# Performance work log

Measured on AMD Instinct MI355X. Metric: run time of the kernel, lower is better.

Reference implementation:

```python
import jax, jax.numpy as jnp
import numpy as np

T, B, N, L = 4, 8, 25000, 64
D_IN = 1 + 2 * L  # node_dim + latent + time_dim


def setup_inputs() -> dict:
    key = jax.random.key(0)
    ks = jax.random.split(key, 20)
    f = lambda k, shp, s=0.1: jax.random.normal(k, shp, dtype=jnp.float32) * s
    z = lambda shp: jnp.zeros(shp, jnp.float32)
    return dict(
        raw=f(ks[0], (T, B, N, 1), 1.0),
        r_label=f(ks[1], (T, B, N, 1), 1.0),
        t=jax.random.uniform(ks[2], (T, B, N, 1), dtype=jnp.float32) * 100.0,
        src=jax.random.randint(ks[3], (T, B), 0, N, dtype=jnp.int32),
        tar=jax.random.randint(ks[4], (T, B), 0, N, dtype=jnp.int32),
        n_mask=jax.random.randint(ks[5], (T, B, N), 0, 2, dtype=jnp.int32),
        w_t=f(ks[6], (L,)), b_t=f(ks[7], (L,)),
        W_msg=f(ks[8], (1 + L, L)), b_msg=z((L,)),
        Wi=f(ks[9], (L, 3 * L)), Wh=f(ks[10], (L, 3 * L)),
        bi=z((3 * L,)), bh=z((3 * L,)),
        Wq=f(ks[11], (D_IN, L)), bq=z((L,)),
        Wk=f(ks[12], (D_IN, L)), bk=z((L,)),
        Wv=f(ks[13], (D_IN, L)), bv=z((L,)),
        W_out=f(ks[14], (L, 1)), b_out=z((1,)),
    )


def reference(raw, r_label, t, src, tar, n_mask, w_t, b_t, W_msg, b_msg,
              Wi, Wh, bi, bh, Wq, bq, Wk, bk, Wv, bv, W_out, b_out):
    Ldim = w_t.shape[0]
    Bdim, Ndim = raw.shape[1], raw.shape[2]
    bidx = jnp.arange(Bdim)
    scale = 1.0 / jnp.sqrt(jnp.float32(Ldim))
    enc0 = jnp.cos(b_t)  # time encoding of t=0 for the target query

    def time_enc(tt):  # [..., 1] -> [..., L]
        return jnp.cos(tt * w_t + b_t)

    def gru(x, h):  # torch.nn.GRUCell math
        gi = x @ Wi + bi
        gh = h @ Wh + bh
        ir, iz, inn = jnp.split(gi, 3, axis=-1)
        hr, hz, hn = jnp.split(gh, 3, axis=-1)
        rg = jax.nn.sigmoid(ir + hr)
        zg = jax.nn.sigmoid(iz + hz)
        ng = jnp.tanh(inn + rg * hn)
        return (1.0 - zg) * ng + zg * h

    def step(carry, inp):
        memory, r = carry            # [N,L], [B,N,1]
        t_b, tar_b, mask_b, rlab_b = inp  # [B,N,1], [B], [B,N], [N,1]
        enc_t = time_enc(t_b)        # [B,N,L]
        # 1. memory update (message from last batch element, GRU over all nodes)
        msg = jnp.concatenate([r[-1], enc_t[-1]], axis=-1) @ W_msg + b_msg  # [N,L]
        mem2 = gru(msg, memory)      # [N,L]
        # 2. embedding: target query over all node features
        tar_r = r[bidx, tar_b]       # [B,1]
        tar_hid = mem2[tar_b]        # [B,L]
        tar_h = jnp.concatenate(
            [tar_r, tar_hid, jnp.broadcast_to(enc0, (Bdim, Ldim))], axis=-1)  # [B,1+2L]
        h = jnp.concatenate(
            [r, jnp.broadcast_to(mem2[None], (Bdim, Ndim, Ldim)), enc_t], axis=-1)  # [B,N,1+2L]
        q = tar_h @ Wq + bq          # [B,L]
        k = h @ Wk + bk              # [B,N,L]
        v = h @ Wv + bv              # [B,N,L]
        scores = jnp.einsum('bl,bnl->bn', q, k) * scale
        scores = jnp.where(mask_b > 0, scores, jnp.float32(-1e9))
        attn = jax.nn.softmax(scores, axis=-1)
        z = jnp.einsum('bn,bnl->bl', attn, v)  # [B,L]
        logit = z @ W_out + b_out    # [B,1]
        # vectorized scatter replacing the python loop r_pred[tar_id]=pred_logit
        r_pred = r[-1].at[tar_b].set(logit)    # [N,1]
        r_last = 0.5 * (r_pred + rlab_b)       # teacher forcing blend
        r_next = jnp.broadcast_to(r_last[None], (Bdim, Ndim, 1))
        return (mem2, r_next), logit

    mem0 = jnp.zeros((Ndim, Ldim), jnp.float32)
    rlab_last = r_label[:, -1]  # [T,N,1]
    (_, _), logits = jax.lax.scan(step, (mem0, raw[0]), (t, tar, n_mask, rlab_last))
    return logits  # [T,B,1]
```

## Files before the change

### kernel.cpp

```cpp
#include <hip/hip_runtime.h>
#include <math.h>

#define TSTEPS 4
#define BB 8
#define NN 25000
#define LLD 64
#define DIN 129

#define OFF_W6    0
#define OFF_I4    24576
#define OFF_R4    24832
#define OFF_A     25088
#define OFF_WQ0   33473
#define OFF_CA    33602
#define OFF_C0Q   33667
#define OFF_WVO   33668
#define OFF_C0    33797
#define OFF_WQC   33856
#define OFF_BFRAG 36864
#define OFF_MEMA  73728
#define OFF_MEMB  1673728
#define OFF_RLAST 3273728
#define OFF_PART  3298728
#define NBLK 98
#define PSTRIDE 132

typedef short s16x8 __attribute__((ext_vector_type(8)));
typedef float f32x4 __attribute__((ext_vector_type(4)));

__device__ __forceinline__ float sigm(float x) { return 1.f / (1.f + __expf(-x)); }
__device__ __forceinline__ float tanh_fast(float x) {
  float ax = fabsf(x);
  float e = __expf(-2.f * ax);
  float t = (1.f - e) / (1.f + e);
  return copysignf(t, x);
}
__device__ __forceinline__ float wred_max(float v) {
#pragma unroll
  for (int m = 32; m; m >>= 1) v = fmaxf(v, __shfl_xor(v, m));
  return v;
}
__device__ __forceinline__ float wred_sum(float v) {
#pragma unroll
  for (int m = 32; m; m >>= 1) v += __shfl_xor(v, m);
  return v;
}
__device__ __forceinline__ unsigned short bf16_rne(float v) {
  unsigned int u = __float_as_uint(v);
  unsigned int r = (u + 0x7FFFu + ((u >> 16) & 1u)) >> 16;
  return (unsigned short)r;
}
__device__ __forceinline__ float bf16_to_f(unsigned short b) {
  return __uint_as_float(((unsigned int)b) << 16);
}

__global__ __launch_bounds__(1024) void k_setup(
    const float* __restrict__ W_msg, const float* __restrict__ Wi,
    const float* __restrict__ bi, const float* __restrict__ b_msg,
    const float* __restrict__ bh, const float* __restrict__ Wh,
    const float* __restrict__ Wq, const float* __restrict__ bq,
    const float* __restrict__ Wk, const float* __restrict__ bk,
    const float* __restrict__ Wv, const float* __restrict__ bv,
    const float* __restrict__ W_out, const float* __restrict__ b_out,
    const float* __restrict__ b_t, float* __restrict__ ws) {
  if (blockIdx.x == 0) {
    __shared__ float u_lds[64];
    int tid = threadIdx.x;
    if (tid < 64) {
      float acc = bq[tid];
      for (int l = 0; l < 64; l++) acc += __cosf(b_t[l]) * Wq[(65 + l) * 64 + tid];
      u_lds[tid] = acc;
    }
    __syncthreads();
    if (tid < 129) {
      float acc = 0.f;
      for (int j = 0; j < 64; j++) acc += Wk[tid * 64 + j] * u_lds[j];
      ws[OFF_WQ0 + tid] = acc;
    } else if (tid == 129) {
      float acc = 0.f;
      for (int j = 0; j < 64; j++) acc += bk[j] * u_lds[j];
      ws[OFF_C0Q] = acc;
    }
    return;
  }
  int id = (blockIdx.x - 1) * 1024 + threadIdx.x;
  if (id < 24576) {
    int k = id / 384, rem = id % 384, l = rem / 6, g = rem % 6;
    float acc = 0.f;
    if (g < 3) {
      for (int m = 0; m < 64; m++) acc += W_msg[(k + 1) * 64 + m] * Wi[m * 192 + g * 64 + l];
    } else {
      acc = Wh[k * 192 + (g - 3) * 64 + l];
    }
    ws[OFF_W6 + id] = acc;
  } else if (id < 24832) {
    int id2 = id - 24576, l = id2 / 4, g = id2 % 4;
    float v;
    if (g == 3) v = bh[128 + l];
    else {
      int j = g * 64 + l;
      float bcf = bi[j];
      for (int m = 0; m < 64; m++) bcf += b_msg[m] * Wi[m * 192 + j];
      v = (g < 2) ? (bcf + bh[j]) : bcf;
    }
    ws[OFF_I4 + id2] = v;
  } else if (id < 25088) {
    int id2 = id - 24832, l = id2 / 4, g = id2 % 4;
    float v = 0.f;
    if (g < 3) {
      for (int m = 0; m < 64; m++) v += W_msg[m] * Wi[m * 192 + g * 64 + l];
    }
    ws[OFF_R4 + id2] = v;
  } else if (id < 33473) {
    int id3 = id - 25088, d = id3 / 65, i = id3 % 65;
    float acc = 0.f;
    for (int j = 0; j < 64; j++) acc += Wk[d * 64 + j] * Wq[i * 64 + j];
    ws[OFF_A + id3] = acc;
  } else if (id < 33538) {
    int i = id - 33473;
    float acc = 0.f;
    for (int j = 0; j < 64; j++) acc += bk[j] * Wq[i * 64 + j];
    ws[OFF_CA + i] = acc;
  } else if (id < 33667) {
    int d = id - 33538;
    float acc = 0.f;
    for (int j = 0; j < 64; j++) acc += Wv[d * 64 + j] * W_out[j];
    ws[OFF_WVO + d] = acc;
  } else if (id == 33667) {
    float acc = b_out[0];
    for (int j = 0; j < 64; j++) acc += bv[j] * W_out[j];
    ws[OFF_C0] = acc;
  }
}

__global__ __launch_bounds__(1024) void k_pack(
    const float* __restrict__ ws_r, float* __restrict__ ws) {
  int id = blockIdx.x * 1024 + threadIdx.x;
  int r = id & 7, lane = (id >> 3) & 63, kt = (id >> 9) & 3, ct = id >> 11;
  int col = 16 * ct + (lane & 15);
  int k = 32 * kt + ((lane >> 4) << 3) + r;
  int a = col >> 6, l = col & 63;
  float w = 0.f;
  if (k < 64) {
    if (a < 3) w = ws_r[OFF_W6 + (k * 64 + l) * 6 + a];
  } else {
    int k2 = k - 64;
    if (a == 0) w = ws_r[OFF_W6 + (k2 * 64 + l) * 6 + 3];
    else if (a == 1) w = ws_r[OFF_W6 + (k2 * 64 + l) * 6 + 4];
    else if (a == 3) w = ws_r[OFF_W6 + (k2 * 64 + l) * 6 + 5];
  }
  unsigned short hb = bf16_rne(w);
  unsigned short lb = bf16_rne(w - bf16_to_f(hb));
  unsigned short* BFu = (unsigned short*)(ws + OFF_BFRAG);
  int idx = ((ct * 4 + kt) * 64 + lane) * 8 + r;
  BFu[idx] = hb;
  BFu[32768 + idx] = lb;
}

__global__ __launch_bounds__(256, 2) void k_gru(
    const float* __restrict__ t_in, const float* __restrict__ raw,
    const float* __restrict__ r_in, const float* __restrict__ w_t,
    const float* __restrict__ b_t, const float* __restrict__ i4p,
    const float* __restrict__ r4p, const unsigned short* __restrict__ BF,
    const float* __restrict__ memPrev, float* __restrict__ memNext,
    const int* __restrict__ tar, const float* __restrict__ A,
    const float* __restrict__ wq0, const float* __restrict__ cA,
    const float* __restrict__ c0q, float* __restrict__ wqc, int tt) {
  __shared__ unsigned short XhiS[64 * 136];
  __shared__ unsigned short XloS[64 * 136];
  __shared__ float tb_lds[64], rn_lds[64];
  __shared__ float q_lds[64];
  int tid = threadIdx.x;
  int lane = tid & 63;
  int wv = tid >> 6;
  int nbase = blockIdx.x * 64;

  if (tid < 64) {
    int nc = min(nbase + tid, NN - 1);
    tb_lds[tid] = t_in[(tt * BB + BB - 1) * NN + nc];
    rn_lds[tid] = (tt == 0) ? raw[(BB - 1) * NN + nc] : r_in[nc];
  }
  __syncthreads();

  {
    int nl = lane;
    int nc = min(nbase + nl, NN - 1);
    float tb = tb_lds[nl];
    int swz = (nl & 7) << 3;
    const float4* mp4 = (const float4*)(memPrev + (size_t)nc * 64);
#pragma unroll
    for (int c = 0; c < 4; c++) {
      int kc = wv * 32 + c * 8;
      float vv[8];
      if (kc < 64) {
#pragma unroll
        for (int j = 0; j < 8; j++) vv[j] = __cosf(tb * w_t[kc + j] + b_t[kc + j]);
      } else if (tt == 0) {
#pragma unroll
        for (int j = 0; j < 8; j++) vv[j] = 0.f;
      } else {
        int d0 = kc - 64;
        float4 f0 = mp4[d0 >> 2];
        float4 f1 = mp4[(d0 >> 2) + 1];
        vv[0] = f0.x; vv[1] = f0.y; vv[2] = f0.z; vv[3] = f0.w;
        vv[4] = f1.x; vv[5] = f1.y; vv[6] = f1.z; vv[7] = f1.w;
      }
      s16x8 h8, l8;
#pragma unroll
      for (int j = 0; j < 8; j++) {
        unsigned short hb = bf16_rne(vv[j]);
        h8[j] = (short)hb;
        l8[j] = (short)bf16_rne(vv[j] - bf16_to_f(hb));
      }
      int off = nl * 136 + (kc ^ swz);
      *(s16x8*)(XhiS + off) = h8;
      *(s16x8*)(XloS + off) = l8;
    }
  }
  __syncthreads();

  const s16x8* BF8 = (const s16x8*)BF;
  f32x4 acc[4][4];
#pragma unroll
  for (int g = 0; g < 4; g++)
#pragma unroll
    for (int m = 0; m < 4; m++) acc[g][m] = (f32x4){0.f, 0.f, 0.f, 0.f};

  int swzA = (lane & 7) << 3;
#pragma unroll
  for (int kt = 0; kt < 4; kt++) {
    s16x8 bh[4], bl[4];
#pragma unroll
    for (int g = 0; g < 4; g++) {
      int ct = wv + 4 * g;
      bh[g] = BF8[(ct * 4 + kt) * 64 + lane];
      bl[g] = BF8[4096 + (ct * 4 + kt) * 64 + lane];
    }
#pragma unroll
    for (int m = 0; m < 4; m++) {
      int row = 16 * m + (lane & 15);
      int off = row * 136 + ((32 * kt + 8 * (lane >> 4)) ^ swzA);
      s16x8 ah = *(const s16x8*)(XhiS + off);
      s16x8 al = *(const s16x8*)(XloS + off);
#pragma unroll
      for (int g = 0; g < 4; g++) {
        acc[g][m] = __builtin_amdgcn_mfma_f32_16x16x32_bf16(ah, bh[g], acc[g][m], 0, 0, 0);
        acc[g][m] = __builtin_amdgcn_mfma_f32_16x16x32_bf16(ah, bl[g], acc[g][m], 0, 0, 0);
        acc[g][m] = __builtin_amdgcn_mfma_f32_16x16x32_bf16(al, bh[g], acc[g][m], 0, 0, 0);
      }
    }
  }

  int myl = 16 * wv + (lane & 15);
  float4 iv = ((const float4*)i4p)[myl];
  float4 rv = ((const float4*)r4p)[myl];
  int kmem = 64 + myl;
  int slot = kmem & ~7;
  int wel = kmem & 7;
#pragma unroll
  for (int m = 0; m < 4; m++) {
#pragma unroll
    for (int i = 0; i < 4; i++) {
      int nloc = 16 * m + (lane >> 4) * 4 + i;
      float rn = rn_lds[nloc];
      float gRv = acc[0][m][i] + iv.x + rn * rv.x;
      float gZv = acc[1][m][i] + iv.y + rn * rv.y;
      float aNv = acc[2][m][i] + iv.z + rn * rv.z;
      float hNv = acc[3][m][i] + iv.w;
      float rg = sigm(gRv);
      float zg = sigm(gZv);
      float ng = tanh_fast(aNv + rg * hNv);
      int offm = nloc * 136 + (slot ^ ((nloc & 7) << 3)) + wel;
      float mp = bf16_to_f(XhiS[offm]) + bf16_to_f(XloS[offm]);
      int n = nbase + nloc;
      if (n < NN) memNext[(size_t)n * 64 + myl] = (1.f - zg) * ng + zg * mp;
    }
  }

  for (int b = 0; b < BB; b++) {
    int tn = tar[tt * BB + b];
    if ((tn >> 6) != (int)blockIdx.x) continue;
    __syncthreads();
    if (tid < 64) q_lds[tid] = memNext[(size_t)tn * 64 + tid];
    __syncthreads();
    float tr = (tt == 0) ? raw[b * NN + tn] : r_in[tn];
    if (tid < 129) {
      const float* Ar = A + tid * 65;
      float acc2 = wq0[tid] + tr * Ar[0];
#pragma unroll 8
      for (int k = 0; k < 64; k++) acc2 += q_lds[k] * Ar[1 + k];
      wqc[b * 132 + tid] = acc2;
    } else if (tid == 129) {
      float acc2 = c0q[0] + tr * cA[0];
      for (int k = 0; k < 64; k++) acc2 += q_lds[k] * cA[1 + k];
      wqc[b * 132 + 129] = acc2;
    }
    __syncthreads();
  }
}

__global__ __launch_bounds__(256) void k_attn(
    const float* __restrict__ t_in, const float* __restrict__ raw,
    const float* __restrict__ r_last, const int* __restrict__ n_mask,
    const float* __restrict__ w_t, const float* __restrict__ b_t,
    const float* __restrict__ wqc, const float* __restrict__ mem2,
    float* __restrict__ part, int tt) {
  __shared__ float wq_lds[132];
  __shared__ float e_sh[256], t_sh[256];
  __shared__ float red4[4], redS[4], redR[4];
  __shared__ float pmw[4][64], pew[4][64];

  int tid = threadIdx.x;
  int lane = tid & 63;
  int wvid = tid >> 6;
  int b = blockIdx.y;
  int n0 = blockIdx.x * 256;
  int n = n0 + tid;
  int nc = min(n, NN - 1);
  bool valid = (n < NN);

  if (tid < 130) wq_lds[tid] = wqc[b * 132 + tid];

  float tb = t_in[(tt * BB + b) * NN + nc];
  int mk = n_mask[(tt * BB + b) * NN + nc];
  float rn = (tt == 0) ? raw[b * NN + nc] : r_last[nc];
  __syncthreads();

  float sc = rn * wq_lds[0];
  const float4* m4 = (const float4*)(mem2 + (size_t)nc * 64);
#pragma unroll
  for (int q = 0; q < 16; q++) {
    float4 v = m4[q];
    sc += v.x * wq_lds[1 + 4 * q] + v.y * wq_lds[2 + 4 * q] +
          v.z * wq_lds[3 + 4 * q] + v.w * wq_lds[4 + 4 * q];
  }
#pragma unroll 8
  for (int l = 0; l < 64; l++) sc += __cosf(tb * w_t[l] + b_t[l]) * wq_lds[65 + l];
  float score = (sc + wq_lds[129]) * 0.125f;
  bool act = valid && (mk > 0);

  float mw = wred_max(act ? score : -1e30f);
  if (lane == 0) red4[wvid] = mw;
  __syncthreads();
  float mb = fmaxf(fmaxf(red4[0], red4[1]), fmaxf(red4[2], red4[3]));

  float e = act ? __expf(score - mb) : 0.f;
  float sw = wred_sum(e);
  float sr = wred_sum(e * rn);
  if (lane == 0) { redS[wvid] = sw; redR[wvid] = sr; }
  e_sh[tid] = e;
  t_sh[tid] = tb;
  __syncthreads();
  float Sb = redS[0] + redS[1] + redS[2] + redS[3];
  float Rb = redR[0] + redR[1] + redR[2] + redR[3];

  {
    int ib = wvid * 64;
    float a0 = 0.f, a1 = 0.f, a2 = 0.f, a3 = 0.f;
    float a4 = 0.f, a5 = 0.f, a6 = 0.f, a7 = 0.f;
#pragma unroll 2
    for (int i = 0; i < 64; i += 8) {
      int i0 = ib + i;
      a0 += e_sh[i0 + 0] * mem2[(size_t)min(n0 + i0 + 0, NN - 1) * 64 + lane];
      a1 += e_sh[i0 + 1] * mem2[(size_t)min(n0 + i0 + 1, NN - 1) * 64 + lane];
      a2 += e_sh[i0 + 2] * mem2[(size_t)min(n0 + i0 + 2, NN - 1) * 64 + lane];
      a3 += e_sh[i0 + 3] * mem2[(size_t)min(n0 + i0 + 3, NN - 1) * 64 + lane];
      a4 += e_sh[i0 + 4] * mem2[(size_t)min(n0 + i0 + 4, NN - 1) * 64 + lane];
      a5 += e_sh[i0 + 5] * mem2[(size_t)min(n0 + i0 + 5, NN - 1) * 64 + lane];
      a6 += e_sh[i0 + 6] * mem2[(size_t)min(n0 + i0 + 6, NN - 1) * 64 + lane];
      a7 += e_sh[i0 + 7] * mem2[(size_t)min(n0 + i0 + 7, NN - 1) * 64 + lane];
    }
    pmw[wvid][lane] = ((a0 + a1) + (a2 + a3)) + ((a4 + a5) + (a6 + a7));
    float wl = w_t[lane], bl = b_t[lane];
    float peA = 0.f;
#pragma unroll 4
    for (int i = 0; i < 64; i++) peA += e_sh[ib + i] * __cosf(t_sh[ib + i] * wl + bl);
    pew[wvid][lane] = peA;
  }
  __syncthreads();

  int pbase = (b * NBLK + blockIdx.x) * PSTRIDE;
  if (tid < 64) part[pbase + 1 + tid] = (pmw[0][tid] + pmw[1][tid]) + (pmw[2][tid] + pmw[3][tid]);
  else if (tid < 128) {
    int d = tid - 64;
    part[pbase + 65 + d] = (pew[0][d] + pew[1][d]) + (pew[2][d] + pew[3][d]);
  }
  else if (tid == 128) part[pbase + 0] = Rb;
  else if (tid == 129) part[pbase + 129] = mb;
  else if (tid == 130) part[pbase + 130] = Sb;
}

__global__ __launch_bounds__(256) void k_merge(
    const float* __restrict__ part, const float* __restrict__ wvo,
    const float* __restrict__ c0p, const int* __restrict__ tar,
    const float* __restrict__ raw, const float* __restrict__ r_label,
    float* __restrict__ r_last, float* __restrict__ out, int tt) {
  int tid = threadIdx.x;
  if (blockIdx.x < NBLK) {
    int n = blockIdx.x * 256 + tid;
    if (n >= NN) return;
    bool istar = false;
#pragma unroll
    for (int b = 0; b < BB; b++) istar |= (tar[tt * BB + b] == n);
    if (istar) return;
    float base = (tt == 0) ? raw[(BB - 1) * NN + n] : r_last[n];
    r_last[n] = 0.5f * (base + r_label[(tt * BB + BB - 1) * NN + n]);
    return;
  }

  int b = blockIdx.x - NBLK;
  const float* pb = part + b * NBLK * PSTRIDE;
  __shared__ float red[256], fac[NBLK];

  red[tid] = (tid < NBLK) ? pb[tid * PSTRIDE + 129] : -1e30f;
  __syncthreads();
  for (int s = 128; s > 0; s >>= 1) {
    if (tid < s) red[tid] = fmaxf(red[tid], red[tid + s]);
    __syncthreads();
  }
  float mb = red[0];
  __syncthreads();
  if (tid < NBLK) fac[tid] = __expf(pb[tid * PSTRIDE + 129] - mb);
  __syncthreads();
  red[tid] = (tid < NBLK) ? pb[tid * PSTRIDE + 130] * fac[tid] : 0.f;
  __syncthreads();
  for (int s = 128; s > 0; s >>= 1) {
    if (tid < s) red[tid] += red[tid + s];
    __syncthreads();
  }
  float Sb = red[0];
  __syncthreads();

  float acc = 0.f;
  if (tid < DIN) {
    float a0 = 0.f, a1 = 0.f, a2 = 0.f, a3 = 0.f;
    int j = 0;
    for (; j + 3 < NBLK; j += 4) {
      a0 += fac[j] * pb[j * PSTRIDE + tid];
      a1 += fac[j + 1] * pb[(j + 1) * PSTRIDE + tid];
      a2 += fac[j + 2] * pb[(j + 2) * PSTRIDE + tid];
      a3 += fac[j + 3] * pb[(j + 3) * PSTRIDE + tid];
    }
    for (; j < NBLK; j++) a0 += fac[j] * pb[j * PSTRIDE + tid];
    acc = ((a0 + a1) + (a2 + a3)) * wvo[tid];
  }
  red[tid] = (tid < DIN) ? acc : 0.f;
  __syncthreads();
  for (int s = 128; s > 0; s >>= 1) {
    if (tid < s) red[tid] += red[tid + s];
    __syncthreads();
  }
  if (tid == 0) {
    float lg = red[0] / Sb + c0p[0];
    out[tt * BB + b] = lg;
    int mytar = tar[tt * BB + b];
    bool last = true;
    for (int bb = b + 1; bb < BB; bb++)
      if (tar[tt * BB + bb] == mytar) last = false;
    if (last)
      r_last[mytar] = 0.5f * (lg + r_label[(tt * BB + BB - 1) * NN + mytar]);
  }
}

extern "C" void kernel_launch(void* const* d_in, const int* in_sizes, int n_in,
                              void* d_out, int out_size, void* d_ws, size_t ws_size,
                              hipStream_t stream) {
  const float* raw     = (const float*)d_in[0];
  const float* r_label = (const float*)d_in[1];
  const float* t_in    = (const float*)d_in[2];
  const int*   tar     = (const int*)d_in[4];
  const int*   n_mask  = (const int*)d_in[5];
  const float* w_t     = (const float*)d_in[6];
  const float* b_t     = (const float*)d_in[7];
  const float* W_msg   = (const float*)d_in[8];
  const float* b_msg   = (const float*)d_in[9];
  const float* Wi      = (const float*)d_in[10];
  const float* Wh      = (const float*)d_in[11];
  const float* bi      = (const float*)d_in[12];
  const float* bh      = (const float*)d_in[13];
  const float* Wq      = (const float*)d_in[14];
  const float* bq      = (const float*)d_in[15];
  const float* Wk      = (const float*)d_in[16];
  const float* bk      = (const float*)d_in[17];
  const float* Wv      = (const float*)d_in[18];
  const float* bv      = (const float*)d_in[19];
  const float* W_out   = (const float*)d_in[20];
  const float* b_out   = (const float*)d_in[21];

  float* ws  = (float*)d_ws;
  float* out = (float*)d_out;

  k_setup<<<34, 1024, 0, stream>>>(W_msg, Wi, bi, b_msg, bh, Wh, Wq, bq, Wk, bk,
                                   Wv, bv, W_out, b_out, b_t, ws);
  k_pack<<<32, 1024, 0, stream>>>(ws, ws);

  for (int tt = 0; tt < TSTEPS; tt++) {
    float* mp = ws + ((tt & 1) ? OFF_MEMB : OFF_MEMA);
    float* mn = ws + ((tt & 1) ? OFF_MEMA : OFF_MEMB);
    k_gru<<<dim3((NN + 63) / 64), dim3(256), 0, stream>>>(
        t_in, raw, ws + OFF_RLAST, w_t, b_t,
        ws + OFF_I4, ws + OFF_R4, (const unsigned short*)(ws + OFF_BFRAG),
        mp, mn, tar, ws + OFF_A, ws + OFF_WQ0, ws + OFF_CA, ws + OFF_C0Q,
        ws + OFF_WQC, tt);
    k_attn<<<dim3(NBLK, BB), dim3(256), 0, stream>>>(
        t_in, raw, ws + OFF_RLAST, n_mask, w_t, b_t,
        ws + OFF_WQC, mn, ws + OFF_PART, tt);
    k_merge<<<dim3(NBLK + BB), dim3(256), 0, stream>>>(
        ws + OFF_PART, ws + OFF_WVO, ws + OFF_C0, tar,
        raw, r_label, ws + OFF_RLAST, out, tt);
  }
}
```

Baseline: 182.1 us.

## Fuse per-step merge and r_last update into next step's GRU kernel

Removes the separate k_merge launch per timestep by folding the softmax-partial merge, logit output and teacher-forcing r_last update into the start of the following k_gru launch. Only the final step keeps a small k_fin kernel. This saves three kernel launches and their inter-kernel gaps, at the cost of extra shared memory and serialized merge work in the GRU blocks that own target nodes. When two batch entries share a target, the blend order now follows batch order (last one wins), replacing the earlier explicit last-writer check.

```diff
diff --git a/kernel.cpp b/kernel.cpp
--- a/kernel.cpp
+++ b/kernel.cpp
@@ -157,28 +157,105 @@
   BFu[32768 + idx] = lb;
 }
 
+__device__ __forceinline__ float merge_logit(
+    const float* __restrict__ pb, const float* __restrict__ wvo,
+    float c0v, float* __restrict__ red, float* __restrict__ fac, int tid) {
+  red[tid] = (tid < NBLK) ? pb[tid * PSTRIDE + 129] : -1e30f;
+  __syncthreads();
+  for (int s = 128; s > 0; s >>= 1) {
+    if (tid < s) red[tid] = fmaxf(red[tid], red[tid + s]);
+    __syncthreads();
+  }
+  float mb = red[0];
+  __syncthreads();
+  if (tid < NBLK) fac[tid] = __expf(pb[tid * PSTRIDE + 129] - mb);
+  __syncthreads();
+  red[tid] = (tid < NBLK) ? pb[tid * PSTRIDE + 130] * fac[tid] : 0.f;
+  __syncthreads();
+  for (int s = 128; s > 0; s >>= 1) {
+    if (tid < s) red[tid] += red[tid + s];
+    __syncthreads();
+  }
+  float Sb = red[0];
+  __syncthreads();
+  float acc = 0.f;
+  if (tid < DIN) {
+    float a0 = 0.f, a1 = 0.f, a2 = 0.f, a3 = 0.f;
+    int j = 0;
+    for (; j + 3 < NBLK; j += 4) {
+      a0 += fac[j] * pb[j * PSTRIDE + tid];
+      a1 += fac[j + 1] * pb[(j + 1) * PSTRIDE + tid];
+      a2 += fac[j + 2] * pb[(j + 2) * PSTRIDE + tid];
+      a3 += fac[j + 3] * pb[(j + 3) * PSTRIDE + tid];
+    }
+    for (; j < NBLK; j++) a0 += fac[j] * pb[j * PSTRIDE + tid];
+    acc = ((a0 + a1) + (a2 + a3)) * wvo[tid];
+  }
+  red[tid] = (tid < DIN) ? acc : 0.f;
+  __syncthreads();
+  for (int s = 128; s > 0; s >>= 1) {
+    if (tid < s) red[tid] += red[tid + s];
+    __syncthreads();
+  }
+  float lg = red[0] / Sb + c0v;
+  __syncthreads();
+  return lg;
+}
+
 __global__ __launch_bounds__(256, 2) void k_gru(
     const float* __restrict__ t_in, const float* __restrict__ raw,
-    const float* __restrict__ r_in, const float* __restrict__ w_t,
+    float* __restrict__ r_last, const float* __restrict__ w_t,
     const float* __restrict__ b_t, const float* __restrict__ i4p,
     const float* __restrict__ r4p, const unsigned short* __restrict__ BF,
     const float* __restrict__ memPrev, float* __restrict__ memNext,
     const int* __restrict__ tar, const float* __restrict__ A,
     const float* __restrict__ wq0, const float* __restrict__ cA,
-    const float* __restrict__ c0q, float* __restrict__ wqc, int tt) {
+    const float* __restrict__ c0q, float* __restrict__ wqc,
+    const float* __restrict__ part, const float* __restrict__ wvo,
+    const float* __restrict__ c0p, const float* __restrict__ r_label,
+    float* __restrict__ out, int tt) {
   __shared__ unsigned short XhiS[64 * 136];
   __shared__ unsigned short XloS[64 * 136];
   __shared__ float tb_lds[64], rn_lds[64];
   __shared__ float q_lds[64];
+  __shared__ float mred[256], mfac[NBLK];
   int tid = threadIdx.x;
   int lane = tid & 63;
   int wv = tid >> 6;
   int nbase = blockIdx.x * 64;
 
+  if (tt > 0) {
+    int ptt = tt - 1;
+    if (tid < 64) {
+      int n2 = nbase + tid;
+      if (n2 < NN) {
+        bool istar = false;
+#pragma unroll
+        for (int b = 0; b < BB; b++) istar |= (tar[ptt * BB + b] == n2);
+        if (!istar) {
+          float base = (ptt == 0) ? raw[(BB - 1) * NN + n2] : r_last[n2];
+          r_last[n2] = 0.5f * (base + r_label[(ptt * BB + BB - 1) * NN + n2]);
+        }
+      }
+    }
+    __syncthreads();
+    for (int b = 0; b < BB; b++) {
+      int tn = tar[ptt * BB + b];
+      if ((tn >> 6) != (int)blockIdx.x) continue;
+      float lg = merge_logit(part + b * NBLK * PSTRIDE, wvo, c0p[0], mred, mfac, tid);
+      if (tid == 0) {
+        out[ptt * BB + b] = lg;
+        r_last[tn] = 0.5f * (lg + r_label[(ptt * BB + BB - 1) * NN + tn]);
+      }
+      __syncthreads();
+    }
+    __syncthreads();
+  }
+
   if (tid < 64) {
     int nc = min(nbase + tid, NN - 1);
     tb_lds[tid] = t_in[(tt * BB + BB - 1) * NN + nc];
-    rn_lds[tid] = (tt == 0) ? raw[(BB - 1) * NN + nc] : r_in[nc];
+    rn_lds[tid] = (tt == 0) ? raw[(BB - 1) * NN + nc] : r_last[nc];
   }
   __syncthreads();
 
@@ -283,7 +360,7 @@
     __syncthreads();
     if (tid < 64) q_lds[tid] = memNext[(size_t)tn * 64 + tid];
     __syncthreads();
-    float tr = (tt == 0) ? raw[b * NN + tn] : r_in[tn];
+    float tr = (tt == 0) ? raw[b * NN + tn] : r_last[tn];
     if (tid < 129) {
       const float* Ar = A + tid * 65;
       float acc2 = wq0[tid] + tr * Ar[0];
@@ -390,76 +467,14 @@
   else if (tid == 130) part[pbase + 130] = Sb;
 }
 
-__global__ __launch_bounds__(256) void k_merge(
+__global__ __launch_bounds__(256) void k_fin(
     const float* __restrict__ part, const float* __restrict__ wvo,
-    const float* __restrict__ c0p, const int* __restrict__ tar,
-    const float* __restrict__ raw, const float* __restrict__ r_label,
-    float* __restrict__ r_last, float* __restrict__ out, int tt) {
+    const float* __restrict__ c0p, float* __restrict__ out, int tt) {
+  __shared__ float red[256], fac[NBLK];
   int tid = threadIdx.x;
-  if (blockIdx.x < NBLK) {
-    int n = blockIdx.x * 256 + tid;
-    if (n >= NN) return;
-    bool istar = false;
-#pragma unroll
-    for (int b = 0; b < BB; b++) istar |= (tar[tt * BB + b] == n);
-    if (istar) return;
-    float base = (tt == 0) ? raw[(BB - 1) * NN + n] : r_last[n];
-    r_last[n] = 0.5f * (base + r_label[(tt * BB + BB - 1) * NN + n]);
-    return;
-  }
-
-  int b = blockIdx.x - NBLK;
-  const float* pb = part + b * NBLK * PSTRIDE;
-  __shared__ float red[256], fac[NBLK];
-
-  red[tid] = (tid < NBLK) ? pb[tid * PSTRIDE + 129] : -1e30f;
-  __syncthreads();
-  for (int s = 128; s > 0; s >>= 1) {
-    if (tid < s) red[tid] = fmaxf(red[tid], red[tid + s]);
-    __syncthreads();
-  }
-  float mb = red[0];
-  __syncthreads();
-  if (tid < NBLK) fac[tid] = __expf(pb[tid * PSTRIDE + 129] - mb);
-  __syncthreads();
-  red[tid] = (tid < NBLK) ? pb[tid * PSTRIDE + 130] * fac[tid] : 0.f;
-  __syncthreads();
-  for (int s = 128; s > 0; s >>= 1) {
-    if (tid < s) red[tid] += red[tid + s];
-    __syncthreads();
-  }
-  float Sb = red[0];
-  __syncthreads();
-
-  float acc = 0.f;
-  if (tid < DIN) {
-    float a0 = 0.f, a1 = 0.f, a2 = 0.f, a3 = 0.f;
-    int j = 0;
-    for (; j + 3 < NBLK; j += 4) {
-      a0 += fac[j] * pb[j * PSTRIDE + tid];
-      a1 += fac[j + 1] * pb[(j + 1) * PSTRIDE + tid];
-      a2 += fac[j + 2] * pb[(j + 2) * PSTRIDE + tid];
-      a3 += fac[j + 3] * pb[(j + 3) * PSTRIDE + tid];
-    }
-    for (; j < NBLK; j++) a0 += fac[j] * pb[j * PSTRIDE + tid];
-    acc = ((a0 + a1) + (a2 + a3)) * wvo[tid];
-  }
-  red[tid] = (tid < DIN) ? acc : 0.f;
-  __syncthreads();
-  for (int s = 128; s > 0; s >>= 1) {
-    if (tid < s) red[tid] += red[tid + s];
-    __syncthreads();
-  }
-  if (tid == 0) {
-    float lg = red[0] / Sb + c0p[0];
-    out[tt * BB + b] = lg;
-    int mytar = tar[tt * BB + b];
-    bool last = true;
-    for (int bb = b + 1; bb < BB; bb++)
-      if (tar[tt * BB + bb] == mytar) last = false;
-    if (last)
-      r_last[mytar] = 0.5f * (lg + r_label[(tt * BB + BB - 1) * NN + mytar]);
-  }
+  int b = blockIdx.x;
+  float lg = merge_logit(part + b * NBLK * PSTRIDE, wvo, c0p[0], red, fac, tid);
+  if (tid == 0) out[tt * BB + b] = lg;
 }
 
 extern "C" void kernel_launch(void* const* d_in, const int* in_sizes, int n_in,
@@ -501,12 +516,12 @@
         t_in, raw, ws + OFF_RLAST, w_t, b_t,
         ws + OFF_I4, ws + OFF_R4, (const unsigned short*)(ws + OFF_BFRAG),
         mp, mn, tar, ws + OFF_A, ws + OFF_WQ0, ws + OFF_CA, ws + OFF_C0Q,
-        ws + OFF_WQC, tt);
+        ws + OFF_WQC, ws + OFF_PART, ws + OFF_WVO, ws + OFF_C0,
+        r_label, out, tt);
     k_attn<<<dim3(NBLK, BB), dim3(256), 0, stream>>>(
         t_in, raw, ws + OFF_RLAST, n_mask, w_t, b_t,
         ws + OFF_WQC, mn, ws + OFF_PART, tt);
-    k_merge<<<dim3(NBLK + BB), dim3(256), 0, stream>>>(
-        ws + OFF_PART, ws + OFF_WVO, ws + OFF_C0, tar,
-        raw, r_label, ws + OFF_RLAST, out, tt);
-  }
-}
+  }
+  k_fin<<<dim3(BB), dim3(256), 0, stream>>>(
+      ws + OFF_PART, ws + OFF_WVO, ws + OFF_C0, out, TSTEPS - 1);
+}
```

After: 170.9 us (median of 2 runs). 1.07x faster.
